# Kernel tuning notes

Hardware: AMD Instinct MI355X
Metric: run time of the kernel (lower is better)

## Reference

```python
import jax, jax.numpy as jnp
import numpy as np

B, L, M = 256, 8, 1024  # batch, input_length (= window), latent dim m
P = 8                   # predict_length


def setup_inputs() -> dict:
    key = jax.random.key(0)
    k1, k2, k3 = jax.random.split(key, 3)
    x = jax.random.normal(k1, (B, L, M), dtype=jnp.float32)
    # A initialized near identity (original init is torch.eye repeated), plus
    # small noise so the test is non-trivial and the recurrence stays stable.
    eye = jnp.broadcast_to(jnp.eye(M, dtype=jnp.float32), (L, M, M))
    A_real = eye / L + 0.02 * jax.random.normal(k2, (L, M, M), dtype=jnp.float32)
    A_imag = 0.02 * jax.random.normal(k3, (L, M, M), dtype=jnp.float32)
    return {"x": x, "A_real": A_real, "A_imag": A_imag, "predict_length": P}


def reference(x, A_real, A_imag, predict_length):
    # Complex DMD operator bank: A[j] is [M, M] cfloat.
    A = (A_real + 1j * A_imag).astype(jnp.complex64)
    Lw = x.shape[1]
    # Original inner loop: u2 += A[j] @ uc[:, -j]  (note -0 == 0!)
    #   j=0 pairs A[0] with window position 0; j>=1 pairs A[j] with position Lw-j.
    # Re-index so term for window position p uses Ag[p]: Ag[0]=A[0], Ag[p]=A[Lw-p].
    idx = jnp.concatenate([jnp.array([0]), jnp.arange(Lw - 1, 0, -1)])
    Ag = A[idx]  # [Lw, M, M]

    uc0 = x.astype(jnp.complex64)  # [B, Lw, M] sliding window state

    def step(uc, _):
        # Fused accumulation: sum_p Ag[p] @ uc[:, p]  -> [B, M]
        u2 = jnp.einsum("kmn,bkn->bm", Ag, uc)
        uc = jnp.concatenate([uc[:, 1:], u2[:, None]], axis=1)  # slide window
        return uc, None

    uc, _ = jax.lax.scan(step, uc0, None, length=predict_length)
    # Original casts cfloat -> double, which drops the imaginary part; keep fp32.
    return jnp.real(uc).astype(jnp.float32)
```

## Files before the change

kernel.cpp:

```cpp
#include <hip/hip_runtime.h>


#define LW 8

typedef __attribute__((ext_vector_type(8))) short  short8;
typedef __attribute__((ext_vector_type(8))) __bf16 bf16x8;
typedef __attribute__((ext_vector_type(4))) float  f32x4;
typedef __attribute__((ext_vector_type(4))) float  f4;
typedef const __attribute__((address_space(1))) void gvoid_t;
typedef __attribute__((address_space(3))) void lvoid_t;

static __device__ __forceinline__ short f2bf(float f) {
  unsigned u = __builtin_bit_cast(unsigned, f);
  u += 0x7FFFu + ((u >> 16) & 1u);
  return (short)(u >> 16);
}
static __device__ __forceinline__ float bf2f(short s) {
  unsigned u = ((unsigned)(unsigned short)s) << 16;
  return __builtin_bit_cast(float, u);
}
static __device__ __forceinline__ f32x4 mfma16(short8 a, short8 b, f32x4 c) {
  return __builtin_amdgcn_mfma_f32_16x16x32_bf16(
      __builtin_bit_cast(bf16x8, a), __builtin_bit_cast(bf16x8, b), c, 0, 0, 0);
}

__global__ __launch_bounds__(1024) void prep_s(const float* __restrict__ x,
                                               short* __restrict__ Sr2,
                                               short* __restrict__ Si2) {
  const int tg = blockIdx.x * 1024 + threadIdx.x;
  const int qn = tg & 3, kc = (tg >> 2) & 31, b = (tg >> 7) & 255, s = tg >> 15;
  const float* xp = x + ((size_t)(b * LW + s) << 10) + (kc << 5) + (qn << 3);
  f4 x0 = *(const f4*)xp, x1 = *(const f4*)(xp + 4);
  short8 v;
#pragma unroll
  for (int j = 0; j < 4; ++j) { v[j] = f2bf(x0[j]); v[j + 4] = f2bf(x1[j]); }
  const int sq = qn ^ ((b >> 1) & 3);
  const size_t dst = ((size_t)s << 18) + (kc << 13) + (b << 5) + (sq << 3);
  *(short8*)(Sr2 + dst) = v;
  short8 z = {0, 0, 0, 0, 0, 0, 0, 0};
  *(short8*)(Si2 + dst) = z;
}

__global__ __launch_bounds__(1024) void prep_w(const float* __restrict__ Ar,
                                               const float* __restrict__ Ai,
                                               short* __restrict__ WTr,
                                               short* __restrict__ WTi) {
  const int tg = blockIdx.x * 1024 + threadIdx.x;
  const int sq = tg & 3, col = (tg >> 2) & 63, kcg = (tg >> 8) & 31;
  const int colt = (tg >> 13) & 15, p = tg >> 17;
  const int qn = sq ^ ((col >> 1) & 3);
  const int m = (colt << 6) + col, n0 = (kcg << 5) + (qn << 3);
  const int qm = (LW - p) & 7;
  const size_t src = ((size_t)((qm << 10) + m) << 10) + n0;
  f4 r0 = *(const f4*)(Ar + src), r1 = *(const f4*)(Ar + src + 4);
  f4 i0 = *(const f4*)(Ai + src), i1 = *(const f4*)(Ai + src + 4);
  short8 vr, vi;
#pragma unroll
  for (int j = 0; j < 4; ++j) {
    vr[j] = f2bf(r0[j]); vr[j + 4] = f2bf(r1[j]);
    vi[j] = f2bf(i0[j]); vi[j + 4] = f2bf(i1[j]);
  }
  *(short8*)(WTr + ((size_t)tg << 3)) = vr;
  *(short8*)(WTi + ((size_t)tg << 3)) = vi;
}


#define LOADA(set_, kc_) do {                                                    \
    const int kg_ = ((ks << 3) + (kc_)) << 13;                                   \
    _Pragma("unroll")                                                            \
    for (int rf_ = 0; rf_ < 4; ++rf_) {                                          \
      aR[set_][rf_] = *(const short8*)(SrB + kg_ + aoffG[rf_]);                  \
      aI[set_][rf_] = *(const short8*)(SiB + kg_ + aoffG[rf_]);                  \
    }                                                                            \
  } while (0)

#define COMP(set_, kc_) do {                                                     \
    short8 bR_[4], bI_[4];                                                       \
    _Pragma("unroll")                                                            \
    for (int cf_ = 0; cf_ < 4; ++cf_) {                                          \
      bR_[cf_] = *(const short8*)(ldsW + ((kc_) << 11) + boffL[cf_]);            \
      bI_[cf_] = *(const short8*)(ldsW + 16384 + ((kc_) << 11) + boffL[cf_]);    \
    }                                                                            \
    _Pragma("unroll")                                                            \
    for (int rf_ = 0; rf_ < 4; ++rf_) {                                          \
      const short8 nI_ = aI[set_][rf_] ^ SGN;                                    \
      _Pragma("unroll")                                                          \
      for (int cf_ = 0; cf_ < 4; ++cf_) {                                        \
        accR[rf_][cf_] = mfma16(aR[set_][rf_], bR_[cf_], accR[rf_][cf_]);        \
        accR[rf_][cf_] = mfma16(nI_,           bI_[cf_], accR[rf_][cf_]);        \
        accI[rf_][cf_] = mfma16(aR[set_][rf_], bI_[cf_], accI[rf_][cf_]);        \
        accI[rf_][cf_] = mfma16(aI[set_][rf_], bR_[cf_], accI[rf_][cf_]);        \
      }                                                                          \
    }                                                                            \
  } while (0)

__global__ __launch_bounds__(256, 2) void gemm_step(const short* __restrict__ Sr2,
                                                    const short* __restrict__ Si2,
                                                    const short* __restrict__ WTr,
                                                    const short* __restrict__ WTi,
                                                    short* __restrict__ Pp,
                                                    int t) {
  __shared__ short ldsW[32768];

  const int bid   = blockIdx.x;
  const int p     = bid & 7;
  const int inner = bid >> 3;
  const int colt  = inner & 15;
  const int ks    = inner >> 4;
  const int s     = (p + t) & 7;

  const int tid = threadIdx.x, lane = tid & 63, w = tid >> 6;
  const int l15 = lane & 15, q = lane >> 4;

  {
    const short* baseR = WTr + (((size_t)((p << 4) + colt)) << 16) + ((size_t)(ks << 3) << 11);
    const short* baseI = WTi + (((size_t)((p << 4) + colt)) << 16) + ((size_t)(ks << 3) << 11);
#pragma unroll
    for (int j = 0; j < 16; ++j) {
      const int gid  = (j << 8) + tid;
      const int arr  = gid >> 11;
      const int rem  = gid & 2047;
      const short* src = (arr ? baseI : baseR) + (rem << 3);
      __builtin_amdgcn_global_load_lds((gvoid_t*)src,
          (lvoid_t*)&ldsW[(arr << 14) + (rem << 3)], 16, 0, 0);
    }
  }

  const short* SrB = Sr2 + ((size_t)s << 18);
  const short* SiB = Si2 + ((size_t)s << 18);
  int aoffG[4], boffL[4];
#pragma unroll
  for (int rf = 0; rf < 4; ++rf) {
    const int row = (w << 6) + (rf << 4) + l15;
    aoffG[rf] = (row << 5) + ((q ^ ((row >> 1) & 3)) << 3);
  }
#pragma unroll
  for (int cf = 0; cf < 4; ++cf) {
    const int col = (cf << 4) + l15;
    boffL[cf] = (col << 5) + ((q ^ ((col >> 1) & 3)) << 3);
  }

  f32x4 accR[4][4], accI[4][4];
  const f32x4 z4 = {0.f, 0.f, 0.f, 0.f};
#pragma unroll
  for (int a = 0; a < 4; ++a)
#pragma unroll
    for (int c = 0; c < 4; ++c) { accR[a][c] = z4; accI[a][c] = z4; }

  const short8 SGN = {(short)0x8000, (short)0x8000, (short)0x8000, (short)0x8000,
                      (short)0x8000, (short)0x8000, (short)0x8000, (short)0x8000};

  short8 aR[2][4], aI[2][4];

  LOADA(0, 0);
  __syncthreads();

#pragma unroll
  for (int kc = 0; kc < 8; ++kc) {
    if (kc < 7) LOADA((kc + 1) & 1, kc + 1);
    COMP(kc & 1, kc);
  }

  short* op = Pp + ((size_t)((((((p << 2) + ks) << 4) + colt) << 4)) << 11) + (tid << 3);
#pragma unroll
  for (int rf = 0; rf < 4; ++rf)
#pragma unroll
    for (int cf = 0; cf < 4; ++cf) {
      short8 sv;
#pragma unroll
      for (int rg = 0; rg < 4; ++rg) {
        sv[rg]     = f2bf(accR[rf][cf][rg]);
        sv[rg + 4] = f2bf(accI[rf][cf][rg]);
      }
      *(short8*)(op + ((size_t)((rf << 2) + cf) << 11)) = sv;
    }
}

__global__ __launch_bounds__(256) void reduce_step(const short* __restrict__ Pp,
                                                   short* __restrict__ Sr2,
                                                   short* __restrict__ Si2,
                                                   float* __restrict__ out,
                                                   int t) {
  const int r = blockIdx.x * 256 + threadIdx.x;
  const int tidg = r & 255, o = (r >> 8) & 15, colt = r >> 12;

  float sum[8] = {0.f, 0.f, 0.f, 0.f, 0.f, 0.f, 0.f, 0.f};
#pragma unroll
  for (int sl = 0; sl < 32; ++sl) {
    const short8 v = *(const short8*)(
        Pp + ((size_t)sl << 19) + ((size_t)colt << 15) + (o << 11) + (tidg << 3));
#pragma unroll
    for (int jj = 0; jj < 8; ++jj) sum[jj] += bf2f(v[jj]);
  }

  const int rf = o >> 2, cf = o & 3;
  const int lane = tidg & 63, w = tidg >> 6;
  const int l15 = lane & 15, q = lane >> 4;
  const int row0 = (w << 6) + (rf << 4) + (q << 2);
  const int col  = (colt << 6) + (cf << 4) + l15;
  const int kc = col >> 5, qn = (col >> 3) & 3, j = col & 7;

#pragma unroll
  for (int rg = 0; rg < 4; ++rg) {
    const int row = row0 + rg;
    out[((size_t)((row << 3) + t) << 10) + col] = sum[rg];
    const int sq = qn ^ ((row >> 1) & 3);
    const size_t idx = ((size_t)t << 18) + (kc << 13) + (row << 5) + (sq << 3) + j;
    Sr2[idx] = f2bf(sum[rg]);
    Si2[idx] = f2bf(sum[rg + 4]);
  }
}

extern "C" void kernel_launch(void* const* d_in, const int* in_sizes, int n_in,
                              void* d_out, int out_size, void* d_ws, size_t ws_size,
                              hipStream_t stream) {
  const float* x  = (const float*)d_in[0];
  const float* Ar = (const float*)d_in[1];
  const float* Ai = (const float*)d_in[2];
  float* out = (float*)d_out;

  char* ws = (char*)d_ws;
  if (ws_size < (80u << 20)) return;
  short* Sr2 = (short*)(ws);
  short* Si2 = (short*)(ws + (4u  << 20));
  short* WTr = (short*)(ws + (8u  << 20));
  short* WTi = (short*)(ws + (24u << 20));
  short* Pp  = (short*)(ws + (40u << 20));

  prep_w<<<dim3(1024), dim3(1024), 0, stream>>>(Ar, Ai, WTr, WTi);
  prep_s<<<dim3(256), dim3(1024), 0, stream>>>(x, Sr2, Si2);
  for (int t = 0; t < 8; ++t) {
    gemm_step<<<dim3(512), dim3(256), 0, stream>>>(Sr2, Si2, WTr, WTi, Pp, t);
    reduce_step<<<dim3(256), dim3(256), 0, stream>>>(Pp, Sr2, Si2, out, t);
  }
}
```

Measured before the change: 239.2 us.

## Halve K-split and use 512-thread GEMM blocks; merge prep kernels

The GEMM step now splits K into 2 slices instead of 4. Each block runs 8 waves arranged 4x2 over a 256x64 output tile and stages a 64 KB weight slice in LDS. The reduce kernel sums 16 partial slices instead of 32, which cuts partial-sum traffic. The two preprocessing kernels are fused into one launch. The trade-offs are fewer blocks (256), so less parallelism across CUs, and more LDS per block, which may lower occupancy.

```diff
diff --git a/kernel.cpp b/kernel.cpp
--- a/kernel.cpp
+++ b/kernel.cpp
@@ -24,49 +24,51 @@
       __builtin_bit_cast(bf16x8, a), __builtin_bit_cast(bf16x8, b), c, 0, 0, 0);
 }
 
-__global__ __launch_bounds__(1024) void prep_s(const float* __restrict__ x,
-                                               short* __restrict__ Sr2,
-                                               short* __restrict__ Si2) {
-  const int tg = blockIdx.x * 1024 + threadIdx.x;
-  const int qn = tg & 3, kc = (tg >> 2) & 31, b = (tg >> 7) & 255, s = tg >> 15;
-  const float* xp = x + ((size_t)(b * LW + s) << 10) + (kc << 5) + (qn << 3);
-  f4 x0 = *(const f4*)xp, x1 = *(const f4*)(xp + 4);
-  short8 v;
-#pragma unroll
-  for (int j = 0; j < 4; ++j) { v[j] = f2bf(x0[j]); v[j + 4] = f2bf(x1[j]); }
-  const int sq = qn ^ ((b >> 1) & 3);
-  const size_t dst = ((size_t)s << 18) + (kc << 13) + (b << 5) + (sq << 3);
-  *(short8*)(Sr2 + dst) = v;
-  short8 z = {0, 0, 0, 0, 0, 0, 0, 0};
-  *(short8*)(Si2 + dst) = z;
-}
-
-__global__ __launch_bounds__(1024) void prep_w(const float* __restrict__ Ar,
-                                               const float* __restrict__ Ai,
-                                               short* __restrict__ WTr,
-                                               short* __restrict__ WTi) {
-  const int tg = blockIdx.x * 1024 + threadIdx.x;
-  const int sq = tg & 3, col = (tg >> 2) & 63, kcg = (tg >> 8) & 31;
-  const int colt = (tg >> 13) & 15, p = tg >> 17;
-  const int qn = sq ^ ((col >> 1) & 3);
-  const int m = (colt << 6) + col, n0 = (kcg << 5) + (qn << 3);
-  const int qm = (LW - p) & 7;
-  const size_t src = ((size_t)((qm << 10) + m) << 10) + n0;
-  f4 r0 = *(const f4*)(Ar + src), r1 = *(const f4*)(Ar + src + 4);
-  f4 i0 = *(const f4*)(Ai + src), i1 = *(const f4*)(Ai + src + 4);
-  short8 vr, vi;
-#pragma unroll
-  for (int j = 0; j < 4; ++j) {
-    vr[j] = f2bf(r0[j]); vr[j + 4] = f2bf(r1[j]);
-    vi[j] = f2bf(i0[j]); vi[j + 4] = f2bf(i1[j]);
-  }
-  *(short8*)(WTr + ((size_t)tg << 3)) = vr;
-  *(short8*)(WTi + ((size_t)tg << 3)) = vi;
+__global__ __launch_bounds__(1024) void prep_all(const float* __restrict__ x,
+                                                 const float* __restrict__ Ar,
+                                                 const float* __restrict__ Ai,
+                                                 short* __restrict__ Sr2,
+                                                 short* __restrict__ Si2,
+                                                 short* __restrict__ WTr,
+                                                 short* __restrict__ WTi) {
+  const int bid = blockIdx.x;
+  if (bid < 1024) {
+    const int tg = bid * 1024 + threadIdx.x;
+    const int sq = tg & 3, col = (tg >> 2) & 63, kcg = (tg >> 8) & 31;
+    const int colt = (tg >> 13) & 15, p = tg >> 17;
+    const int qn = sq ^ ((col >> 1) & 3);
+    const int m = (colt << 6) + col, n0 = (kcg << 5) + (qn << 3);
+    const int qm = (LW - p) & 7;
+    const size_t src = ((size_t)((qm << 10) + m) << 10) + n0;
+    f4 r0 = *(const f4*)(Ar + src), r1 = *(const f4*)(Ar + src + 4);
+    f4 i0 = *(const f4*)(Ai + src), i1 = *(const f4*)(Ai + src + 4);
+    short8 vr, vi;
+#pragma unroll
+    for (int j = 0; j < 4; ++j) {
+      vr[j] = f2bf(r0[j]); vr[j + 4] = f2bf(r1[j]);
+      vi[j] = f2bf(i0[j]); vi[j + 4] = f2bf(i1[j]);
+    }
+    *(short8*)(WTr + ((size_t)tg << 3)) = vr;
+    *(short8*)(WTi + ((size_t)tg << 3)) = vi;
+  } else {
+    const int tg = (bid - 1024) * 1024 + threadIdx.x;
+    const int qn = tg & 3, kc = (tg >> 2) & 31, b = (tg >> 7) & 255, s = tg >> 15;
+    const float* xp = x + ((size_t)(b * LW + s) << 10) + (kc << 5) + (qn << 3);
+    f4 x0 = *(const f4*)xp, x1 = *(const f4*)(xp + 4);
+    short8 v;
+#pragma unroll
+    for (int j = 0; j < 4; ++j) { v[j] = f2bf(x0[j]); v[j + 4] = f2bf(x1[j]); }
+    const int sq = qn ^ ((b >> 1) & 3);
+    const size_t dst = ((size_t)s << 18) + (kc << 13) + (b << 5) + (sq << 3);
+    *(short8*)(Sr2 + dst) = v;
+    short8 z = {0, 0, 0, 0, 0, 0, 0, 0};
+    *(short8*)(Si2 + dst) = z;
+  }
 }
 
 
 #define LOADA(set_, kc_) do {                                                    \
-    const int kg_ = ((ks << 3) + (kc_)) << 13;                                   \
+    const int kg_ = ((ks << 4) + (kc_)) << 13;                                   \
     _Pragma("unroll")                                                            \
     for (int rf_ = 0; rf_ < 4; ++rf_) {                                          \
       aR[set_][rf_] = *(const short8*)(SrB + kg_ + aoffG[rf_]);                  \
@@ -75,17 +77,17 @@
   } while (0)
 
 #define COMP(set_, kc_) do {                                                     \
-    short8 bR_[4], bI_[4];                                                       \
+    short8 bR_[2], bI_[2];                                                       \
     _Pragma("unroll")                                                            \
-    for (int cf_ = 0; cf_ < 4; ++cf_) {                                          \
+    for (int cf_ = 0; cf_ < 2; ++cf_) {                                          \
       bR_[cf_] = *(const short8*)(ldsW + ((kc_) << 11) + boffL[cf_]);            \
-      bI_[cf_] = *(const short8*)(ldsW + 16384 + ((kc_) << 11) + boffL[cf_]);    \
+      bI_[cf_] = *(const short8*)(ldsW + 32768 + ((kc_) << 11) + boffL[cf_]);    \
     }                                                                            \
     _Pragma("unroll")                                                            \
     for (int rf_ = 0; rf_ < 4; ++rf_) {                                          \
       const short8 nI_ = aI[set_][rf_] ^ SGN;                                    \
       _Pragma("unroll")                                                          \
-      for (int cf_ = 0; cf_ < 4; ++cf_) {                                        \
+      for (int cf_ = 0; cf_ < 2; ++cf_) {                                        \
         accR[rf_][cf_] = mfma16(aR[set_][rf_], bR_[cf_], accR[rf_][cf_]);        \
         accR[rf_][cf_] = mfma16(nI_,           bI_[cf_], accR[rf_][cf_]);        \
         accI[rf_][cf_] = mfma16(aR[set_][rf_], bI_[cf_], accI[rf_][cf_]);        \
@@ -94,13 +96,13 @@
     }                                                                            \
   } while (0)
 
-__global__ __launch_bounds__(256, 2) void gemm_step(const short* __restrict__ Sr2,
+__global__ __launch_bounds__(512, 2) void gemm_step(const short* __restrict__ Sr2,
                                                     const short* __restrict__ Si2,
                                                     const short* __restrict__ WTr,
                                                     const short* __restrict__ WTi,
                                                     short* __restrict__ Pp,
                                                     int t) {
-  __shared__ short ldsW[32768];
+  __shared__ short ldsW[65536];
 
   const int bid   = blockIdx.x;
   const int p     = bid & 7;
@@ -110,42 +112,43 @@
   const int s     = (p + t) & 7;
 
   const int tid = threadIdx.x, lane = tid & 63, w = tid >> 6;
+  const int rw = w >> 1, cw = w & 1;
   const int l15 = lane & 15, q = lane >> 4;
 
   {
-    const short* baseR = WTr + (((size_t)((p << 4) + colt)) << 16) + ((size_t)(ks << 3) << 11);
-    const short* baseI = WTi + (((size_t)((p << 4) + colt)) << 16) + ((size_t)(ks << 3) << 11);
+    const short* baseR = WTr + (((size_t)((p << 4) + colt)) << 16) + ((size_t)ks << 15);
+    const short* baseI = WTi + (((size_t)((p << 4) + colt)) << 16) + ((size_t)ks << 15);
 #pragma unroll
     for (int j = 0; j < 16; ++j) {
-      const int gid  = (j << 8) + tid;
-      const int arr  = gid >> 11;
-      const int rem  = gid & 2047;
+      const int gid  = (j << 9) + tid;
+      const int arr  = gid >> 12;
+      const int rem  = gid & 4095;
       const short* src = (arr ? baseI : baseR) + (rem << 3);
       __builtin_amdgcn_global_load_lds((gvoid_t*)src,
-          (lvoid_t*)&ldsW[(arr << 14) + (rem << 3)], 16, 0, 0);
+          (lvoid_t*)&ldsW[(arr << 15) + (rem << 3)], 16, 0, 0);
     }
   }
 
   const short* SrB = Sr2 + ((size_t)s << 18);
   const short* SiB = Si2 + ((size_t)s << 18);
-  int aoffG[4], boffL[4];
+  int aoffG[4], boffL[2];
 #pragma unroll
   for (int rf = 0; rf < 4; ++rf) {
-    const int row = (w << 6) + (rf << 4) + l15;
+    const int row = (rw << 6) + (rf << 4) + l15;
     aoffG[rf] = (row << 5) + ((q ^ ((row >> 1) & 3)) << 3);
   }
 #pragma unroll
-  for (int cf = 0; cf < 4; ++cf) {
-    const int col = (cf << 4) + l15;
+  for (int cf = 0; cf < 2; ++cf) {
+    const int col = (cw << 5) + (cf << 4) + l15;
     boffL[cf] = (col << 5) + ((q ^ ((col >> 1) & 3)) << 3);
   }
 
-  f32x4 accR[4][4], accI[4][4];
+  f32x4 accR[4][2], accI[4][2];
   const f32x4 z4 = {0.f, 0.f, 0.f, 0.f};
 #pragma unroll
   for (int a = 0; a < 4; ++a)
 #pragma unroll
-    for (int c = 0; c < 4; ++c) { accR[a][c] = z4; accI[a][c] = z4; }
+    for (int c = 0; c < 2; ++c) { accR[a][c] = z4; accI[a][c] = z4; }
 
   const short8 SGN = {(short)0x8000, (short)0x8000, (short)0x8000, (short)0x8000,
                       (short)0x8000, (short)0x8000, (short)0x8000, (short)0x8000};
@@ -156,23 +159,23 @@
   __syncthreads();
 
 #pragma unroll
-  for (int kc = 0; kc < 8; ++kc) {
-    if (kc < 7) LOADA((kc + 1) & 1, kc + 1);
+  for (int kc = 0; kc < 16; ++kc) {
+    if (kc < 15) LOADA((kc + 1) & 1, kc + 1);
     COMP(kc & 1, kc);
   }
 
-  short* op = Pp + ((size_t)((((((p << 2) + ks) << 4) + colt) << 4)) << 11) + (tid << 3);
+  short* op = Pp + ((size_t)((((p << 1) + ks) << 4) + colt) << 15) + (tid << 3);
 #pragma unroll
   for (int rf = 0; rf < 4; ++rf)
 #pragma unroll
-    for (int cf = 0; cf < 4; ++cf) {
+    for (int cf = 0; cf < 2; ++cf) {
       short8 sv;
 #pragma unroll
       for (int rg = 0; rg < 4; ++rg) {
         sv[rg]     = f2bf(accR[rf][cf][rg]);
         sv[rg + 4] = f2bf(accI[rf][cf][rg]);
       }
-      *(short8*)(op + ((size_t)((rf << 2) + cf) << 11)) = sv;
+      *(short8*)(op + ((size_t)((rf << 1) + cf) << 12)) = sv;
     }
 }
 
@@ -182,22 +185,23 @@
                                                    float* __restrict__ out,
                                                    int t) {
   const int r = blockIdx.x * 256 + threadIdx.x;
-  const int tidg = r & 255, o = (r >> 8) & 15, colt = r >> 12;
+  const int tidg = r & 511, o = (r >> 9) & 7, colt = r >> 12;
 
   float sum[8] = {0.f, 0.f, 0.f, 0.f, 0.f, 0.f, 0.f, 0.f};
 #pragma unroll
-  for (int sl = 0; sl < 32; ++sl) {
+  for (int sl = 0; sl < 16; ++sl) {
     const short8 v = *(const short8*)(
-        Pp + ((size_t)sl << 19) + ((size_t)colt << 15) + (o << 11) + (tidg << 3));
+        Pp + ((size_t)(((sl << 4) + colt) << 3) + o << 12) + (tidg << 3));
 #pragma unroll
     for (int jj = 0; jj < 8; ++jj) sum[jj] += bf2f(v[jj]);
   }
 
-  const int rf = o >> 2, cf = o & 3;
+  const int rf = o >> 1, cf = o & 1;
   const int lane = tidg & 63, w = tidg >> 6;
+  const int rw = w >> 1, cw = w & 1;
   const int l15 = lane & 15, q = lane >> 4;
-  const int row0 = (w << 6) + (rf << 4) + (q << 2);
-  const int col  = (colt << 6) + (cf << 4) + l15;
+  const int row0 = (rw << 6) + (rf << 4) + (q << 2);
+  const int col  = (colt << 6) + (cw << 5) + (cf << 4) + l15;
   const int kc = col >> 5, qn = (col >> 3) & 3, j = col & 7;
 
 #pragma unroll
@@ -220,17 +224,16 @@
   float* out = (float*)d_out;
 
   char* ws = (char*)d_ws;
-  if (ws_size < (80u << 20)) return;
+  if (ws_size < (60u << 20)) return;
   short* Sr2 = (short*)(ws);
   short* Si2 = (short*)(ws + (4u  << 20));
   short* WTr = (short*)(ws + (8u  << 20));
   short* WTi = (short*)(ws + (24u << 20));
   short* Pp  = (short*)(ws + (40u << 20));
 
-  prep_w<<<dim3(1024), dim3(1024), 0, stream>>>(Ar, Ai, WTr, WTi);
-  prep_s<<<dim3(256), dim3(1024), 0, stream>>>(x, Sr2, Si2);
+  prep_all<<<dim3(1280), dim3(1024), 0, stream>>>(x, Ar, Ai, Sr2, Si2, WTr, WTi);
   for (int t = 0; t < 8; ++t) {
-    gemm_step<<<dim3(512), dim3(256), 0, stream>>>(Sr2, Si2, WTr, WTi, Pp, t);
+    gemm_step<<<dim3(256), dim3(512), 0, stream>>>(Sr2, Si2, WTr, WTi, Pp, t);
     reduce_step<<<dim3(256), dim3(256), 0, stream>>>(Pp, Sr2, Si2, out, t);
   }
 }
```

Result: no change. 240.8 us (+0.7%).
